# Performance work log

Measured on AMD Instinct MI355X. Metric: run time of the kernel, lower is better.

Reference implementation:

```python
import jax, jax.numpy as jnp
import numpy as np

N_NODES = 50000
N_EDGES = 500000
IN_DIM = 512
HID = 512


def setup_inputs() -> dict:
    key = jax.random.key(0)
    ks = jax.random.split(key, 12)
    s = 0.02  # weight init scale
    x = jax.random.normal(ks[0], (N_NODES, IN_DIM), dtype=jnp.float32)
    edge_index = jax.random.randint(ks[1], (2, N_EDGES), 0, N_NODES, dtype=jnp.int32)
    return {
        "x": x,
        "edge_index": edge_index,
        "Wl0": jax.random.normal(ks[2], (IN_DIM, HID), jnp.float32) * s,
        "bl0": jnp.zeros((HID,), jnp.float32),
        "Wr0": jax.random.normal(ks[3], (IN_DIM, HID), jnp.float32) * s,
        "Wl1": jax.random.normal(ks[4], (HID, HID), jnp.float32) * s,
        "bl1": jnp.zeros((HID,), jnp.float32),
        "Wr1": jax.random.normal(ks[5], (HID, HID), jnp.float32) * s,
        "Wv": jax.random.normal(ks[6], (HID, HID), jnp.float32) * s,
        "bv": jnp.zeros((HID,), jnp.float32),
        "Wt": jax.random.normal(ks[7], (HID, HID), jnp.float32) * s,
        "bt": jnp.zeros((HID,), jnp.float32),
    }


def _sage_conv(x, src, dst, Wl, bl, Wr, n_nodes):
    # mean-aggregate source features at target nodes, then dual linear
    msg_sum = jax.ops.segment_sum(x[src], dst, num_segments=n_nodes)  # [N, d]
    deg = jax.ops.segment_sum(jnp.ones_like(dst, dtype=x.dtype), dst, num_segments=n_nodes)
    mean = msg_sum / jnp.maximum(deg, 1.0)[:, None]
    return mean @ Wl + bl + x @ Wr


def reference(x, edge_index, Wl0, bl0, Wr0, Wl1, bl1, Wr1, Wv, bv, Wt, bt):
    n = x.shape[0]
    src, dst = edge_index[0], edge_index[1]
    h = _sage_conv(x, src, dst, Wl0, bl0, Wr0, n)
    h = jax.nn.relu(h)  # dropout is identity in eval mode
    h = _sage_conv(h, src, dst, Wl1, bl1, Wr1, n)
    x_vision = jax.nn.relu(h @ Wv + bv)
    x_text = jax.nn.relu(h @ Wt + bt)
    return (h, x_vision, x_text)
```

## Files before the change

### kernel.cpp

```cpp
#include <hip/hip_runtime.h>
#include <hip/hip_bf16.h>
#include <stdint.h>

#define N_NODES 50000
#define N_EDGES 500000
#define DIM 512

typedef unsigned short u16;
typedef unsigned int u32;
typedef __bf16 bf16x8 __attribute__((ext_vector_type(8)));
typedef float f32x4 __attribute__((ext_vector_type(4)));

static __device__ __forceinline__ u16 f2bf(float f) {
  union { __bf16 b; u16 u; } cv; cv.b = (__bf16)f; return cv.u;
}
static __device__ __forceinline__ float bf2f(u16 u) {
  union { u16 u; __bf16 b; } cv; cv.u = u; return (float)cv.b;
}

__global__ void k_hist(const int* __restrict__ dst, int* __restrict__ deg) {
  int e = blockIdx.x * blockDim.x + threadIdx.x;
  if (e < N_EDGES) atomicAdd(&deg[dst[e]], 1);
}

__global__ __launch_bounds__(1024) void k_scan(const int* __restrict__ deg,
                                               int* __restrict__ offs,
                                               int* __restrict__ pos,
                                               float* __restrict__ invd) {
  __shared__ int sums[1024];
  const int tid = threadIdx.x;
  const int CH = 49;
  int lo = tid * CH;
  int hi = lo + CH; if (hi > N_NODES) hi = N_NODES;
  if (lo > N_NODES) lo = N_NODES;
  int s = 0;
  for (int i = lo; i < hi; ++i) s += deg[i];
  sums[tid] = s;
  __syncthreads();
  for (int off = 1; off < 1024; off <<= 1) {
    int t = (tid >= off) ? sums[tid - off] : 0;
    __syncthreads();
    sums[tid] += t;
    __syncthreads();
  }
  int run = sums[tid] - s;
  for (int i = lo; i < hi; ++i) {
    int d = deg[i];
    offs[i] = run; pos[i] = run;
    invd[i] = 1.0f / (float)((d > 1) ? d : 1);
    run += d;
  }
  if (tid == 1023) offs[N_NODES] = run;
}

__global__ void k_scatter(const int* __restrict__ src, const int* __restrict__ dst,
                          int* __restrict__ pos, int* __restrict__ srcs) {
  int e = blockIdx.x * blockDim.x + threadIdx.x;
  if (e < N_EDGES) {
    int p = atomicAdd(&pos[dst[e]], 1);
    srcs[p] = src[e];
  }
}

__global__ void k_cvt_x(const float* __restrict__ x, u16* __restrict__ xb) {
  int t = blockIdx.x * blockDim.x + threadIdx.x;
  const float4* p = (const float4*)(x + (size_t)t * 8);
  float4 a = p[0], b = p[1];
  uint4 o;
  o.x = (u32)f2bf(a.x) | ((u32)f2bf(a.y) << 16);
  o.y = (u32)f2bf(a.z) | ((u32)f2bf(a.w) << 16);
  o.z = (u32)f2bf(b.x) | ((u32)f2bf(b.y) << 16);
  o.w = (u32)f2bf(b.z) | ((u32)f2bf(b.w) << 16);
  *(uint4*)(xb + (size_t)t * 8) = o;
}

__global__ __launch_bounds__(256) void k_cvt_w6(
    const float* __restrict__ Wa, const float* __restrict__ Wb,
    const float* __restrict__ Wc, const float* __restrict__ Wd,
    const float* __restrict__ We, const float* __restrict__ Wf,
    u16* __restrict__ Oa, u16* __restrict__ Ob, u16* __restrict__ Oc,
    u16* __restrict__ Od, u16* __restrict__ Oe, u16* __restrict__ Of) {
  __shared__ u16 tbuf[64][66];
  const float* W; u16* O;
  switch (blockIdx.z) {
    case 0: W = Wa; O = Oa; break;
    case 1: W = Wb; O = Ob; break;
    case 2: W = Wc; O = Oc; break;
    case 3: W = Wd; O = Od; break;
    case 4: W = We; O = Oe; break;
    default: W = Wf; O = Of; break;
  }
  int k0 = blockIdx.x * 64, n0 = blockIdx.y * 64;
  int lr = threadIdx.x & 63, wr = threadIdx.x >> 6;
#pragma unroll
  for (int rr = 0; rr < 16; ++rr) {
    int k = k0 + wr * 16 + rr;
    tbuf[lr][wr * 16 + rr] = f2bf(W[(size_t)k * 512 + n0 + lr]);
  }
  __syncthreads();
#pragma unroll
  for (int rr = 0; rr < 16; ++rr) {
    int n = n0 + wr * 16 + rr;
    O[(size_t)n * 512 + k0 + lr] = tbuf[wr * 16 + rr][lr];
  }
}

__global__ __launch_bounds__(256) void k_agg_bf16(
    const u16* __restrict__ hb, const int* __restrict__ offs,
    const int* __restrict__ srcs, const float* __restrict__ invd,
    u16* __restrict__ outb) {
  int node = blockIdx.x * 4 + (threadIdx.x >> 6);
  int lane = threadIdx.x & 63;
  if (node >= N_NODES) return;
  int s0 = offs[node], s1 = offs[node + 1];
  float acc[8] = {0, 0, 0, 0, 0, 0, 0, 0};
  int i = s0;
  for (; i + 2 <= s1; i += 2) {
    int sa = srcs[i], sb = srcs[i + 1];
    uint4 qa = *(const uint4*)(hb + (size_t)sa * DIM + lane * 8);
    uint4 qb = *(const uint4*)(hb + (size_t)sb * DIM + lane * 8);
    acc[0] += bf2f(qa.x & 0xffff) + bf2f(qb.x & 0xffff);
    acc[1] += bf2f((u16)(qa.x >> 16)) + bf2f((u16)(qb.x >> 16));
    acc[2] += bf2f(qa.y & 0xffff) + bf2f(qb.y & 0xffff);
    acc[3] += bf2f((u16)(qa.y >> 16)) + bf2f((u16)(qb.y >> 16));
    acc[4] += bf2f(qa.z & 0xffff) + bf2f(qb.z & 0xffff);
    acc[5] += bf2f((u16)(qa.z >> 16)) + bf2f((u16)(qb.z >> 16));
    acc[6] += bf2f(qa.w & 0xffff) + bf2f(qb.w & 0xffff);
    acc[7] += bf2f((u16)(qa.w >> 16)) + bf2f((u16)(qb.w >> 16));
  }
  if (i < s1) {
    int sa = srcs[i];
    uint4 qa = *(const uint4*)(hb + (size_t)sa * DIM + lane * 8);
    acc[0] += bf2f(qa.x & 0xffff); acc[1] += bf2f((u16)(qa.x >> 16));
    acc[2] += bf2f(qa.y & 0xffff); acc[3] += bf2f((u16)(qa.y >> 16));
    acc[4] += bf2f(qa.z & 0xffff); acc[5] += bf2f((u16)(qa.z >> 16));
    acc[6] += bf2f(qa.w & 0xffff); acc[7] += bf2f((u16)(qa.w >> 16));
  }
  float iv = invd[node];
  uint4 o;
  o.x = (u32)f2bf(acc[0] * iv) | ((u32)f2bf(acc[1] * iv) << 16);
  o.y = (u32)f2bf(acc[2] * iv) | ((u32)f2bf(acc[3] * iv) << 16);
  o.z = (u32)f2bf(acc[4] * iv) | ((u32)f2bf(acc[5] * iv) << 16);
  o.w = (u32)f2bf(acc[6] * iv) | ((u32)f2bf(acc[7] * iv) << 16);
  *(uint4*)(outb + (size_t)node * DIM + lane * 8) = o;
}

#define MFMA __builtin_amdgcn_mfma_f32_16x16x32_bf16

template <int EPI>
__global__ __launch_bounds__(512, 2) void k_gemm8(
    const u16* __restrict__ A1, const u16* __restrict__ W1,
    const u16* __restrict__ A2, const u16* __restrict__ W2,
    const float* __restrict__ bias,
    float* __restrict__ outf, u16* __restrict__ outb, int NT) {
  __shared__ u16 lds[4 * 16384];
  const int tid = threadIdx.x;
  const int wid = tid >> 6, lane = tid & 63;
  const int wm = wid >> 2, wn = wid & 3;
  const int row0 = ((int)blockIdx.x >> 1) * 256;
  const int colb = ((int)blockIdx.x & 1) * 256;

  f32x4 acc[8][4];
  const f32x4 z = {0.f, 0.f, 0.f, 0.f};
#pragma unroll
  for (int i = 0; i < 8; ++i)
#pragma unroll
    for (int j = 0; j < 4; ++j) acc[i][j] = z;

  const int lx = lane & 7, ly = lane >> 3;
  const int schunk = lx ^ ly;

  auto stage = [&](int t, int isB, int h) {
    u16* tile = lds + (size_t)(((t & 1) << 1) + isB) * 16384;
    const u16* G = (t < 8) ? (isB ? W1 : A1) : (isB ? W2 : A2);
    const int kofs = ((t & 7) * 64) + schunk * 8;
    const int r0 = isB ? colb : row0;
#pragma unroll
    for (int q = 0; q < 2; ++q) {
      const int srw = q * 64 + wid * 8;
      const int r_w = ((srw >> 4) << 5) + h * 16 + (srw & 15);
      int rg = r0 + r_w + ly;
      if (!isB && rg > N_NODES - 1) rg = N_NODES - 1;
      const u16* g = G + (size_t)rg * 512 + kofs;
      __builtin_amdgcn_global_load_lds(
          (const __attribute__((address_space(1))) void*)g,
          (__attribute__((address_space(3))) void*)(tile + r_w * 64), 16, 0, 0);
    }
  };

  auto rdA = [&](const u16* T_, int ig, int kk) -> bf16x8 {
    const int r = (wm * 8 + ig) * 16 + (lane & 15);
    const int off = ((kk * 4 + (lane >> 4)) ^ (lane & 7)) * 8;
    return *(const bf16x8*)(T_ + r * 64 + off);
  };
  auto rdB = [&](const u16* T_, int jg, int kk) -> bf16x8 {
    const int r = (wn * 4 + jg) * 16 + (lane & 15);
    const int off = ((kk * 4 + (lane >> 4)) ^ (lane & 7)) * 8;
    return *(const bf16x8*)(T_ + r * 64 + off);
  };

  stage(0, 0, 0); stage(0, 1, 0); stage(0, 0, 1); stage(0, 1, 1);

  for (int t = 0; t < NT; ++t) {
    const u16* At = lds + (size_t)((t & 1) << 1) * 16384;
    const u16* Bt = At + 16384;
    const bool more = (t + 1 < NT);
    bf16x8 aF[4][2], bF[2][2];

    asm volatile("s_waitcnt vmcnt(4)" ::: "memory");
    __builtin_amdgcn_s_barrier();
    asm volatile("" ::: "memory");
    if (more) stage(t + 1, 0, 0);
#pragma unroll
    for (int ip = 0; ip < 4; ++ip)
#pragma unroll
      for (int kk = 0; kk < 2; ++kk) aF[ip][kk] = rdA(At, 2 * ip, kk);
#pragma unroll
    for (int jp = 0; jp < 2; ++jp)
#pragma unroll
      for (int kk = 0; kk < 2; ++kk) bF[jp][kk] = rdB(Bt, 2 * jp, kk);
    __builtin_amdgcn_s_setprio(1);
#pragma unroll
    for (int ip = 0; ip < 4; ++ip)
#pragma unroll
      for (int jp = 0; jp < 2; ++jp)
#pragma unroll
        for (int kk = 0; kk < 2; ++kk)
          acc[2 * ip][2 * jp] = MFMA(aF[ip][kk], bF[jp][kk], acc[2 * ip][2 * jp], 0, 0, 0);
    __builtin_amdgcn_s_setprio(0);

    if (more) { asm volatile("s_waitcnt vmcnt(2)" ::: "memory"); }
    else      { asm volatile("s_waitcnt vmcnt(0)" ::: "memory"); }
    __builtin_amdgcn_s_barrier();
    asm volatile("" ::: "memory");
    if (more) stage(t + 1, 1, 0);
#pragma unroll
    for (int jp = 0; jp < 2; ++jp)
#pragma unroll
      for (int kk = 0; kk < 2; ++kk) bF[jp][kk] = rdB(Bt, 2 * jp + 1, kk);
    __builtin_amdgcn_s_setprio(1);
#pragma unroll
    for (int ip = 0; ip < 4; ++ip)
#pragma unroll
      for (int jp = 0; jp < 2; ++jp)
#pragma unroll
        for (int kk = 0; kk < 2; ++kk)
          acc[2 * ip][2 * jp + 1] = MFMA(aF[ip][kk], bF[jp][kk], acc[2 * ip][2 * jp + 1], 0, 0, 0);
    __builtin_amdgcn_s_setprio(0);

    if (more) stage(t + 1, 0, 1);
#pragma unroll
    for (int ip = 0; ip < 4; ++ip)
#pragma unroll
      for (int kk = 0; kk < 2; ++kk) aF[ip][kk] = rdA(At, 2 * ip + 1, kk);
    __builtin_amdgcn_s_setprio(1);
#pragma unroll
    for (int ip = 0; ip < 4; ++ip)
#pragma unroll
      for (int jp = 0; jp < 2; ++jp)
#pragma unroll
        for (int kk = 0; kk < 2; ++kk)
          acc[2 * ip + 1][2 * jp + 1] = MFMA(aF[ip][kk], bF[jp][kk], acc[2 * ip + 1][2 * jp + 1], 0, 0, 0);
    __builtin_amdgcn_s_setprio(0);

    if (more) stage(t + 1, 1, 1);
#pragma unroll
    for (int jp = 0; jp < 2; ++jp)
#pragma unroll
      for (int kk = 0; kk < 2; ++kk) bF[jp][kk] = rdB(Bt, 2 * jp, kk);
    __builtin_amdgcn_s_setprio(1);
#pragma unroll
    for (int ip = 0; ip < 4; ++ip)
#pragma unroll
      for (int jp = 0; jp < 2; ++jp)
#pragma unroll
        for (int kk = 0; kk < 2; ++kk)
          acc[2 * ip + 1][2 * jp] = MFMA(aF[ip][kk], bF[jp][kk], acc[2 * ip + 1][2 * jp], 0, 0, 0);
    __builtin_amdgcn_s_setprio(0);
  }

#pragma unroll
  for (int jg = 0; jg < 4; ++jg) {
    int col = colb + (wn * 4 + jg) * 16 + (lane & 15);
    float bb = bias[col];
#pragma unroll
    for (int ig = 0; ig < 8; ++ig) {
      int rbase = row0 + (wm * 8 + ig) * 16 + (lane >> 4) * 4;
      f32x4 v = acc[ig][jg];
#pragma unroll
      for (int r = 0; r < 4; ++r) {
        int row = rbase + r;
        if (row < N_NODES) {
          float f = v[r] + bb;
          if (EPI == 0) {
            f = fmaxf(f, 0.f);
            outb[(size_t)row * DIM + col] = f2bf(f);
          } else if (EPI == 1) {
            outf[(size_t)row * DIM + col] = f;
            outb[(size_t)row * DIM + col] = f2bf(f);
          } else {
            outf[(size_t)row * DIM + col] = fmaxf(f, 0.f);
          }
        }
      }
    }
  }
}

extern "C" void kernel_launch(void* const* d_in, const int* in_sizes, int n_in,
                              void* d_out, int out_size, void* d_ws, size_t ws_size,
                              hipStream_t stream) {
  (void)in_sizes; (void)n_in; (void)out_size; (void)ws_size;
  const float* x   = (const float*)d_in[0];
  const int*   ei  = (const int*)d_in[1];
  const float* Wl0 = (const float*)d_in[2];
  const float* bl0 = (const float*)d_in[3];
  const float* Wr0 = (const float*)d_in[4];
  const float* Wl1 = (const float*)d_in[5];
  const float* bl1 = (const float*)d_in[6];
  const float* Wr1 = (const float*)d_in[7];
  const float* Wv  = (const float*)d_in[8];
  const float* bv  = (const float*)d_in[9];
  const float* Wt  = (const float*)d_in[10];
  const float* bt  = (const float*)d_in[11];
  const int* srcI = ei;
  const int* dstI = ei + N_EDGES;

  float* out_h = (float*)d_out;
  float* out_v = out_h + (size_t)N_NODES * DIM;
  float* out_t = out_v + (size_t)N_NODES * DIM;
  u16* meanb  = (u16*)out_v;
  u16* hrelub = (u16*)out_t;

  uint8_t* p = (uint8_t*)d_ws;
  auto carve = [&](size_t bytes) -> uint8_t* {
    uint8_t* r = p; p += (bytes + 1023) & ~(size_t)1023; return r;
  };
  int*   deg  = (int*)carve((size_t)N_NODES * 4);
  int*   offs = (int*)carve((size_t)(N_NODES + 1) * 4);
  int*   pos  = (int*)carve((size_t)N_NODES * 4);
  float* invd = (float*)carve((size_t)N_NODES * 4);
  int*   srcs = (int*)carve((size_t)N_EDGES * 4);
  u16* Wl0b = (u16*)carve(512 * 512 * 2);
  u16* Wr0b = (u16*)carve(512 * 512 * 2);
  u16* Wl1b = (u16*)carve(512 * 512 * 2);
  u16* Wr1b = (u16*)carve(512 * 512 * 2);
  u16* Wvb  = (u16*)carve(512 * 512 * 2);
  u16* Wtb  = (u16*)carve(512 * 512 * 2);
  u16* xb   = (u16*)carve((size_t)N_NODES * DIM * 2);

  const int EB = (N_EDGES + 255) / 256;

  hipMemsetAsync(deg, 0, (size_t)N_NODES * 4, stream);
  k_hist<<<EB, 256, 0, stream>>>(dstI, deg);
  k_scan<<<1, 1024, 0, stream>>>(deg, offs, pos, invd);
  k_scatter<<<EB, 256, 0, stream>>>(srcI, dstI, pos, srcs);

  k_cvt_x<<<12500, 256, 0, stream>>>(x, xb);
  k_cvt_w6<<<dim3(8, 8, 6), 256, 0, stream>>>(Wl0, Wr0, Wl1, Wr1, Wv, Wt,
                                              Wl0b, Wr0b, Wl1b, Wr1b, Wvb, Wtb);

  const int GB = 392;

  k_agg_bf16<<<12500, 256, 0, stream>>>(xb, offs, srcs, invd, meanb);
  k_gemm8<0><<<GB, 512, 0, stream>>>(meanb, Wl0b, xb, Wr0b, bl0, nullptr, hrelub, 16);

  k_agg_bf16<<<12500, 256, 0, stream>>>(hrelub, offs, srcs, invd, meanb);
  k_gemm8<1><<<GB, 512, 0, stream>>>(meanb, Wl1b, hrelub, Wr1b, bl1, out_h, xb, 16);

  k_gemm8<2><<<GB, 512, 0, stream>>>(xb, Wvb, nullptr, nullptr, bv, out_v, nullptr, 8);
  k_gemm8<2><<<GB, 512, 0, stream>>>(xb, Wtb, nullptr, nullptr, bt, out_t, nullptr, 8);
}
```

Before: 676.0 us.

## Fuse prep kernels, merge head GEMMs, premultiply source indices, unroll aggregation

New measurement: 668.4 us. Within noise of the previous version (-1.1%).

```diff
diff --git a/kernel.cpp b/kernel.cpp
--- a/kernel.cpp
+++ b/kernel.cpp
@@ -16,11 +16,6 @@
 }
 static __device__ __forceinline__ float bf2f(u16 u) {
   union { u16 u; __bf16 b; } cv; cv.u = u; return (float)cv.b;
-}
-
-__global__ void k_hist(const int* __restrict__ dst, int* __restrict__ deg) {
-  int e = blockIdx.x * blockDim.x + threadIdx.x;
-  if (e < N_EDGES) atomicAdd(&deg[dst[e]], 1);
 }
 
 __global__ __launch_bounds__(1024) void k_scan(const int* __restrict__ deg,
@@ -58,12 +53,21 @@
   int e = blockIdx.x * blockDim.x + threadIdx.x;
   if (e < N_EDGES) {
     int p = atomicAdd(&pos[dst[e]], 1);
-    srcs[p] = src[e];
-  }
-}
-
-__global__ void k_cvt_x(const float* __restrict__ x, u16* __restrict__ xb) {
-  int t = blockIdx.x * blockDim.x + threadIdx.x;
+    srcs[p] = src[e] * DIM;
+  }
+}
+
+__global__ __launch_bounds__(256) void k_prep(
+    const float* __restrict__ x, u16* __restrict__ xb,
+    const int* __restrict__ dst, int* __restrict__ deg,
+    const float* __restrict__ Wa, const float* __restrict__ Wb,
+    const float* __restrict__ Wc, const float* __restrict__ Wd,
+    const float* __restrict__ We, const float* __restrict__ Wf,
+    u16* __restrict__ Oa, u16* __restrict__ Ob, u16* __restrict__ Oc,
+    u16* __restrict__ Od, u16* __restrict__ Oe, u16* __restrict__ Of) {
+  __shared__ u16 tbuf[64][66];
+  const int t = blockIdx.x * 256 + threadIdx.x;
+
   const float4* p = (const float4*)(x + (size_t)t * 8);
   float4 a = p[0], b = p[1];
   uint4 o;
@@ -72,38 +76,42 @@
   o.z = (u32)f2bf(b.x) | ((u32)f2bf(b.y) << 16);
   o.w = (u32)f2bf(b.z) | ((u32)f2bf(b.w) << 16);
   *(uint4*)(xb + (size_t)t * 8) = o;
-}
-
-__global__ __launch_bounds__(256) void k_cvt_w6(
-    const float* __restrict__ Wa, const float* __restrict__ Wb,
-    const float* __restrict__ Wc, const float* __restrict__ Wd,
-    const float* __restrict__ We, const float* __restrict__ Wf,
-    u16* __restrict__ Oa, u16* __restrict__ Ob, u16* __restrict__ Oc,
-    u16* __restrict__ Od, u16* __restrict__ Oe, u16* __restrict__ Of) {
-  __shared__ u16 tbuf[64][66];
-  const float* W; u16* O;
-  switch (blockIdx.z) {
-    case 0: W = Wa; O = Oa; break;
-    case 1: W = Wb; O = Ob; break;
-    case 2: W = Wc; O = Oc; break;
-    case 3: W = Wd; O = Od; break;
-    case 4: W = We; O = Oe; break;
-    default: W = Wf; O = Of; break;
-  }
-  int k0 = blockIdx.x * 64, n0 = blockIdx.y * 64;
-  int lr = threadIdx.x & 63, wr = threadIdx.x >> 6;
-#pragma unroll
-  for (int rr = 0; rr < 16; ++rr) {
-    int k = k0 + wr * 16 + rr;
-    tbuf[lr][wr * 16 + rr] = f2bf(W[(size_t)k * 512 + n0 + lr]);
-  }
-  __syncthreads();
-#pragma unroll
-  for (int rr = 0; rr < 16; ++rr) {
-    int n = n0 + wr * 16 + rr;
-    O[(size_t)n * 512 + k0 + lr] = tbuf[wr * 16 + rr][lr];
-  }
-}
+
+  if (t < N_EDGES) atomicAdd(&deg[dst[t]], 1);
+
+  const int wb = (int)blockIdx.x - (12500 - 384);
+  if (wb >= 0) {
+    const float* W; u16* O;
+    switch (wb / 64) {
+      case 0: W = Wa; O = Oa; break;
+      case 1: W = Wb; O = Ob; break;
+      case 2: W = Wc; O = Oc; break;
+      case 3: W = Wd; O = Od; break;
+      case 4: W = We; O = Oe; break;
+      default: W = Wf; O = Of; break;
+    }
+    const int rem = wb & 63;
+    const int k0 = (rem & 7) * 64, n0 = (rem >> 3) * 64;
+    const int lr = threadIdx.x & 63, wr = threadIdx.x >> 6;
+#pragma unroll
+    for (int rr = 0; rr < 16; ++rr) {
+      int k = k0 + wr * 16 + rr;
+      tbuf[lr][wr * 16 + rr] = f2bf(W[(size_t)k * 512 + n0 + lr]);
+    }
+    __syncthreads();
+#pragma unroll
+    for (int rr = 0; rr < 16; ++rr) {
+      int n = n0 + wr * 16 + rr;
+      O[(size_t)n * 512 + k0 + lr] = tbuf[wr * 16 + rr][lr];
+    }
+  }
+}
+
+#define ACC1(q)                                              \
+  acc[0] += bf2f((q).x & 0xffff); acc[1] += bf2f((u16)((q).x >> 16)); \
+  acc[2] += bf2f((q).y & 0xffff); acc[3] += bf2f((u16)((q).y >> 16)); \
+  acc[4] += bf2f((q).z & 0xffff); acc[5] += bf2f((u16)((q).z >> 16)); \
+  acc[6] += bf2f((q).w & 0xffff); acc[7] += bf2f((u16)((q).w >> 16));
 
 __global__ __launch_bounds__(256) void k_agg_bf16(
     const u16* __restrict__ hb, const int* __restrict__ offs,
@@ -114,27 +122,27 @@
   if (node >= N_NODES) return;
   int s0 = offs[node], s1 = offs[node + 1];
   float acc[8] = {0, 0, 0, 0, 0, 0, 0, 0};
+  const u16* hl = hb + lane * 8;
   int i = s0;
-  for (; i + 2 <= s1; i += 2) {
+  for (; i + 4 <= s1; i += 4) {
+    int sa = srcs[i], sb = srcs[i + 1], sc = srcs[i + 2], sd = srcs[i + 3];
+    uint4 qa = *(const uint4*)(hl + sa);
+    uint4 qb = *(const uint4*)(hl + sb);
+    uint4 qc = *(const uint4*)(hl + sc);
+    uint4 qd = *(const uint4*)(hl + sd);
+    ACC1(qa) ACC1(qb) ACC1(qc) ACC1(qd)
+  }
+  if (i + 2 <= s1) {
     int sa = srcs[i], sb = srcs[i + 1];
-    uint4 qa = *(const uint4*)(hb + (size_t)sa * DIM + lane * 8);
-    uint4 qb = *(const uint4*)(hb + (size_t)sb * DIM + lane * 8);
-    acc[0] += bf2f(qa.x & 0xffff) + bf2f(qb.x & 0xffff);
-    acc[1] += bf2f((u16)(qa.x >> 16)) + bf2f((u16)(qb.x >> 16));
-    acc[2] += bf2f(qa.y & 0xffff) + bf2f(qb.y & 0xffff);
-    acc[3] += bf2f((u16)(qa.y >> 16)) + bf2f((u16)(qb.y >> 16));
-    acc[4] += bf2f(qa.z & 0xffff) + bf2f(qb.z & 0xffff);
-    acc[5] += bf2f((u16)(qa.z >> 16)) + bf2f((u16)(qb.z >> 16));
-    acc[6] += bf2f(qa.w & 0xffff) + bf2f(qb.w & 0xffff);
-    acc[7] += bf2f((u16)(qa.w >> 16)) + bf2f((u16)(qb.w >> 16));
+    uint4 qa = *(const uint4*)(hl + sa);
+    uint4 qb = *(const uint4*)(hl + sb);
+    ACC1(qa) ACC1(qb)
+    i += 2;
   }
   if (i < s1) {
     int sa = srcs[i];
-    uint4 qa = *(const uint4*)(hb + (size_t)sa * DIM + lane * 8);
-    acc[0] += bf2f(qa.x & 0xffff); acc[1] += bf2f((u16)(qa.x >> 16));
-    acc[2] += bf2f(qa.y & 0xffff); acc[3] += bf2f((u16)(qa.y >> 16));
-    acc[4] += bf2f(qa.z & 0xffff); acc[5] += bf2f((u16)(qa.z >> 16));
-    acc[6] += bf2f(qa.w & 0xffff); acc[7] += bf2f((u16)(qa.w >> 16));
+    uint4 qa = *(const uint4*)(hl + sa);
+    ACC1(qa)
   }
   float iv = invd[node];
   uint4 o;
@@ -151,14 +159,23 @@
 __global__ __launch_bounds__(512, 2) void k_gemm8(
     const u16* __restrict__ A1, const u16* __restrict__ W1,
     const u16* __restrict__ A2, const u16* __restrict__ W2,
-    const float* __restrict__ bias,
-    float* __restrict__ outf, u16* __restrict__ outb, int NT) {
+    const float* __restrict__ bias, const float* __restrict__ bias2,
+    float* __restrict__ outf, float* __restrict__ outf2,
+    u16* __restrict__ outb, int NT) {
   __shared__ u16 lds[4 * 16384];
   const int tid = threadIdx.x;
   const int wid = tid >> 6, lane = tid & 63;
   const int wm = wid >> 2, wn = wid & 3;
-  const int row0 = ((int)blockIdx.x >> 1) * 256;
-  const int colb = ((int)blockIdx.x & 1) * 256;
+  int head = 0, row0, colb;
+  if (EPI == 3) {
+    head = ((int)blockIdx.x >> 1) & 1;
+    colb = ((int)blockIdx.x & 1) * 256;
+    row0 = ((int)blockIdx.x >> 2) * 256;
+  } else {
+    row0 = ((int)blockIdx.x >> 1) * 256;
+    colb = ((int)blockIdx.x & 1) * 256;
+  }
+  const u16* Bsrc = (EPI == 3) ? (head ? W2 : W1) : nullptr;
 
   f32x4 acc[8][4];
   const f32x4 z = {0.f, 0.f, 0.f, 0.f};
@@ -172,7 +189,9 @@
 
   auto stage = [&](int t, int isB, int h) {
     u16* tile = lds + (size_t)(((t & 1) << 1) + isB) * 16384;
-    const u16* G = (t < 8) ? (isB ? W1 : A1) : (isB ? W2 : A2);
+    const u16* G;
+    if (EPI == 3) G = isB ? Bsrc : A1;
+    else G = (t < 8) ? (isB ? W1 : A1) : (isB ? W2 : A2);
     const int kofs = ((t & 7) * 64) + schunk * 8;
     const int r0 = isB ? colb : row0;
 #pragma unroll
@@ -279,10 +298,12 @@
     __builtin_amdgcn_s_setprio(0);
   }
 
+  const float* bs = (EPI == 3 && head) ? bias2 : bias;
+  float* of = (EPI == 3 && head) ? outf2 : outf;
 #pragma unroll
   for (int jg = 0; jg < 4; ++jg) {
     int col = colb + (wn * 4 + jg) * 16 + (lane & 15);
-    float bb = bias[col];
+    float bb = bs[col];
 #pragma unroll
     for (int ig = 0; ig < 8; ++ig) {
       int rbase = row0 + (wm * 8 + ig) * 16 + (lane >> 4) * 4;
@@ -299,7 +320,7 @@
             outf[(size_t)row * DIM + col] = f;
             outb[(size_t)row * DIM + col] = f2bf(f);
           } else {
-            outf[(size_t)row * DIM + col] = fmaxf(f, 0.f);
+            of[(size_t)row * DIM + col] = fmaxf(f, 0.f);
           }
         }
       }
@@ -352,22 +373,23 @@
   const int EB = (N_EDGES + 255) / 256;
 
   hipMemsetAsync(deg, 0, (size_t)N_NODES * 4, stream);
-  k_hist<<<EB, 256, 0, stream>>>(dstI, deg);
+
+  k_prep<<<12500, 256, 0, stream>>>(x, xb, dstI, deg,
+                                    Wl0, Wr0, Wl1, Wr1, Wv, Wt,
+                                    Wl0b, Wr0b, Wl1b, Wr1b, Wvb, Wtb);
   k_scan<<<1, 1024, 0, stream>>>(deg, offs, pos, invd);
   k_scatter<<<EB, 256, 0, stream>>>(srcI, dstI, pos, srcs);
 
-  k_cvt_x<<<12500, 256, 0, stream>>>(x, xb);
-  k_cvt_w6<<<dim3(8, 8, 6), 256, 0, stream>>>(Wl0, Wr0, Wl1, Wr1, Wv, Wt,
-                                              Wl0b, Wr0b, Wl1b, Wr1b, Wvb, Wtb);
-
   const int GB = 392;
 
   k_agg_bf16<<<12500, 256, 0, stream>>>(xb, offs, srcs, invd, meanb);
-  k_gemm8<0><<<GB, 512, 0, stream>>>(meanb, Wl0b, xb, Wr0b, bl0, nullptr, hrelub, 16);
+  k_gemm8<0><<<GB, 512, 0, stream>>>(meanb, Wl0b, xb, Wr0b, bl0, nullptr,
+                                     nullptr, nullptr, hrelub, 16);
 
   k_agg_bf16<<<12500, 256, 0, stream>>>(hrelub, offs, srcs, invd, meanb);
-  k_gemm8<1><<<GB, 512, 0, stream>>>(meanb, Wl1b, hrelub, Wr1b, bl1, out_h, xb, 16);
-
-  k_gemm8<2><<<GB, 512, 0, stream>>>(xb, Wvb, nullptr, nullptr, bv, out_v, nullptr, 8);
-  k_gemm8<2><<<GB, 512, 0, stream>>>(xb, Wtb, nullptr, nullptr, bt, out_t, nullptr, 8);
-}
+  k_gemm8<1><<<GB, 512, 0, stream>>>(meanb, Wl1b, hrelub, Wr1b, bl1, nullptr,
+                                     out_h, nullptr, xb, 16);
+
+  k_gemm8<3><<<784, 512, 0, stream>>>(xb, Wvb, nullptr, Wtb, bv, bt,
+                                      out_v, out_t, nullptr, 8);
+}
```
